# Performance work log

Measured on AMD Instinct MI355X. Metric: run time of the kernel, lower is better.

The kernel has to match this reference:

```python
import jax, jax.numpy as jnp
import numpy as np

B, SENSORY, STATE, MOTOR = 4096, 64, 128, 32
ODE_UNFOLDS = 6
EPS = 1e-8
ELAPSED_TIME = 1.0


def setup_inputs() -> dict:
    key = jax.random.key(0)
    ks = jax.random.split(key, 20)
    u = lambda k, shape, lo, hi: jax.random.uniform(k, shape, jnp.float32, lo, hi)
    sign = lambda k, shape: jnp.where(jax.random.bernoulli(k, 0.5, shape), 1.0, -1.0).astype(jnp.float32)
    mask = lambda k, shape: (jax.random.uniform(k, shape) < 0.75).astype(jnp.float32)
    return {
        "inputs": jax.random.normal(ks[0], (B, SENSORY), jnp.float32),
        "states": jax.random.normal(ks[1], (B, STATE), jnp.float32),
        "gleak": u(ks[2], (STATE,), 0.001, 1.0),
        "vleak": u(ks[3], (STATE,), -0.2, 0.2),
        "cm": u(ks[4], (STATE,), 0.4, 0.6),
        "w": u(ks[5], (STATE, STATE), 0.001, 1.0),
        "sigma": u(ks[6], (STATE, STATE), 3.0, 8.0),
        "mu": u(ks[7], (STATE, STATE), 0.3, 0.8),
        "erev": sign(ks[8], (STATE, STATE)),
        "sensory_w": u(ks[9], (SENSORY, STATE), 0.001, 1.0),
        "sensory_sigma": u(ks[10], (SENSORY, STATE), 3.0, 8.0),
        "sensory_mu": u(ks[11], (SENSORY, STATE), 0.3, 0.8),
        "sensory_erev": sign(ks[12], (SENSORY, STATE)),
        "sparsity_mask": mask(ks[13], (STATE, STATE)),
        "sensory_sparsity_mask": mask(ks[14], (SENSORY, STATE)),
        "input_w": jnp.ones((SENSORY,), jnp.float32),
        "input_b": jnp.zeros((SENSORY,), jnp.float32),
        "output_w": jnp.ones((MOTOR,), jnp.float32),
        "output_b": jnp.zeros((MOTOR,), jnp.float32),
    }


def _syn_sigmoid(v_pre, mu, sigma):
    # v_pre: [B, P] -> [B, P, 1]; mu/sigma: [P, S]
    return jax.nn.sigmoid(sigma * (v_pre[..., None] - mu))


def reference(inputs, states, gleak, vleak, cm, w, sigma, mu, erev,
              sensory_w, sensory_sigma, sensory_mu, sensory_erev,
              sparsity_mask, sensory_sparsity_mask,
              input_w, input_b, output_w, output_b):
    # input mapping (affine); make_positive_fn = Identity (explicit constraints)
    x = inputs * input_w + input_b

    # sensory contributions (computed once, shared across unfolds)
    sens_act = sensory_w * _syn_sigmoid(x, sensory_mu, sensory_sigma)  # [B, In, S]
    sens_act = sens_act * sensory_sparsity_mask
    w_num_sensory = jnp.sum(sens_act * sensory_erev, axis=1)  # [B, S]
    w_den_sensory = jnp.sum(sens_act, axis=1)                 # [B, S]

    cm_t = cm / (ELAPSED_TIME / ODE_UNFOLDS)  # [S]

    v_pre = states
    for _ in range(ODE_UNFOLDS):
        w_act = w * _syn_sigmoid(v_pre, mu, sigma)   # [B, S, S]
        w_act = w_act * sparsity_mask
        w_numerator = jnp.sum(w_act * erev, axis=1) + w_num_sensory
        w_denominator = jnp.sum(w_act, axis=1) + w_den_sensory
        numerator = cm_t * v_pre + gleak * vleak + w_numerator
        denominator = cm_t + gleak + w_denominator
        v_pre = numerator / (denominator + EPS)

    # output mapping: slice motor neurons, then affine
    output = v_pre[:, :MOTOR] * output_w + output_b
    return output, v_pre
```

## Files before the change

### kernel.cpp

```cpp
#include <hip/hip_runtime.h>

#define LOG2E 1.4426950408889634f

constexpr int Bsz = 4096, Ssz = 128, Isz = 64, MOTOR = 32;
constexpr int BT = 8, R = 4, NT = 512, NQ = 4;

__global__ void ltc_prep(const float* __restrict__ w, const float* __restrict__ sigma,
                         const float* __restrict__ mu, const float* __restrict__ erev,
                         const float* __restrict__ smask,
                         const float* __restrict__ sw, const float* __restrict__ ssig,
                         const float* __restrict__ smu, const float* __restrict__ serev,
                         const float* __restrict__ ssmask,
                         float4* __restrict__ A4, float4* __restrict__ B4, float4* __restrict__ W4,
                         float4* __restrict__ A4s, float4* __restrict__ B4s, float4* __restrict__ W4s)
{
  int idx = blockIdx.x * blockDim.x + threadIdx.x;
  if (idx < (Ssz / 4) * Ssz) {
    int j4 = idx >> 7, s = idx & 127;
    float4 a, b, wv;
    #pragma unroll
    for (int jj = 0; jj < 4; ++jj) {
      int e = (j4 * 4 + jj) * Ssz + s;
      float sg = sigma[e];
      (&a.x)[jj] = -sg * LOG2E;
      (&b.x)[jj] = sg * mu[e] * LOG2E;
      (&wv.x)[jj] = w[e] * smask[e] * erev[e];
    }
    A4[idx] = a; B4[idx] = b; W4[idx] = wv;
  } else if (idx < (Ssz / 4) * Ssz + (Isz / 4) * Ssz) {
    int k = idx - (Ssz / 4) * Ssz;
    int i4 = k >> 7, s = k & 127;
    float4 a, b, wv;
    #pragma unroll
    for (int jj = 0; jj < 4; ++jj) {
      int e = (i4 * 4 + jj) * Ssz + s;
      float sg = ssig[e];
      (&a.x)[jj] = -sg * LOG2E;
      (&b.x)[jj] = sg * smu[e] * LOG2E;
      (&wv.x)[jj] = sw[e] * ssmask[e] * serev[e];
    }
    A4s[k] = a; B4s[k] = b; W4s[k] = wv;
  }
}

__launch_bounds__(NT, 2)
__global__ void ltc_main(const float* __restrict__ inputs, const float* __restrict__ states,
                         const float* __restrict__ gleak, const float* __restrict__ vleak,
                         const float* __restrict__ cmv,
                         const float* __restrict__ iw, const float* __restrict__ ib,
                         const float* __restrict__ ow, const float* __restrict__ ob,
                         const float4* __restrict__ A4, const float4* __restrict__ B4,
                         const float4* __restrict__ W4,
                         const float4* __restrict__ A4s, const float4* __restrict__ B4s,
                         const float4* __restrict__ W4s,
                         float* __restrict__ out)
{
  __shared__ float vsh[BT][Ssz];
  __shared__ float xsh[BT][Isz];
  __shared__ float redn[NQ][R][Ssz];
  __shared__ float redd[NQ][R][Ssz];

  const int t = threadIdx.x;
  const int s = t & 127;
  const int qt = t >> 7;
  const int b0 = blockIdx.x * BT;

  for (int k = t; k < BT * Isz; k += NT) {
    int r = k >> 6, i = k & 63;
    xsh[r][i] = inputs[(b0 + r) * Isz + i] * iw[i] + ib[i];
  }
  for (int k = t; k < BT * Ssz; k += NT) {
    int r = k >> 7, ss = k & 127;
    vsh[r][ss] = states[(b0 + r) * Ssz + ss];
  }
  const float cmt = cmv[s] * 6.0f;
  const float gl = gleak[s];
  const float gv = gl * vleak[s];
  const float dbase = cmt + gl + 1e-8f;

  float4 ta[8], tb[8], tw[8];
  {
    const float4* Ab = A4 + (qt * 8) * Ssz + s;
    const float4* Bb = B4 + (qt * 8) * Ssz + s;
    const float4* Wb = W4 + (qt * 8) * Ssz + s;
    #pragma unroll
    for (int q = 0; q < 8; ++q) {
      ta[q] = Ab[q * Ssz];
      tb[q] = Bb[q * Ssz];
      tw[q] = Wb[q * Ssz];
    }
  }
  __syncthreads();

  #pragma unroll 1
  for (int cb = 0; cb < BT; cb += R) {
    float sn[R] = {0.f, 0.f, 0.f, 0.f}, sd[R] = {0.f, 0.f, 0.f, 0.f};
    #pragma unroll
    for (int q = 0; q < 4; ++q) {
      int iq = qt * 4 + q;
      float4 a4 = A4s[iq * Ssz + s];
      float4 b4 = B4s[iq * Ssz + s];
      float4 w4 = W4s[iq * Ssz + s];
      float4 xq[R];
      #pragma unroll
      for (int r = 0; r < R; ++r) xq[r] = *(const float4*)&xsh[cb + r][iq * 4];
      #pragma unroll
      for (int jj = 0; jj < 4; ++jj) {
        float av = (&a4.x)[jj], bv = (&b4.x)[jj], wv = (&w4.x)[jj];
        #pragma unroll
        for (int r = 0; r < R; ++r) {
          float arg = fmaf(av, (&xq[r].x)[jj], bv);
          float u = __builtin_amdgcn_exp2f(arg);
          float sig = __builtin_amdgcn_rcpf(1.0f + u);
          sn[r] = fmaf(wv, sig, sn[r]);
          sd[r] = fmaf(fabsf(wv), sig, sd[r]);
        }
      }
    }

    #pragma unroll 1
    for (int it = 0; it < 6; ++it) {
      float num[R], den[R];
      #pragma unroll
      for (int r = 0; r < R; ++r) { num[r] = sn[r]; den[r] = sd[r]; }

      #pragma unroll
      for (int q8 = 0; q8 < 8; ++q8) {
        float4 vc[R];
        #pragma unroll
        for (int r = 0; r < R; ++r) vc[r] = *(const float4*)&vsh[cb + r][qt * 32 + q8 * 4];
        #pragma unroll
        for (int jj = 0; jj < 4; ++jj) {
          float av = (&ta[q8].x)[jj], bv = (&tb[q8].x)[jj], wv = (&tw[q8].x)[jj];
          #pragma unroll
          for (int r = 0; r < R; ++r) {
            float arg = fmaf(av, (&vc[r].x)[jj], bv);
            float u = __builtin_amdgcn_exp2f(arg);
            float sig = __builtin_amdgcn_rcpf(1.0f + u);
            num[r] = fmaf(wv, sig, num[r]);
            den[r] = fmaf(fabsf(wv), sig, den[r]);
          }
        }
      }

      #pragma unroll
      for (int r = 0; r < R; ++r) { redn[qt][r][s] = num[r]; redd[qt][r][s] = den[r]; }
      __syncthreads();
      float fn = redn[0][qt][s] + redn[1][qt][s] + redn[2][qt][s] + redn[3][qt][s];
      float fd = redd[0][qt][s] + redd[1][qt][s] + redd[2][qt][s] + redd[3][qt][s];
      float vo = vsh[cb + qt][s];
      float nn = fmaf(cmt, vo, gv) + fn;
      float dd = dbase + fd;
      vsh[cb + qt][s] = nn * __builtin_amdgcn_rcpf(dd);
      __syncthreads();
    }
  }

  for (int k = t; k < BT * Ssz; k += NT) {
    int r = k >> 7, ss = k & 127;
    out[Bsz * MOTOR + (b0 + r) * Ssz + ss] = vsh[r][ss];
  }
  for (int k = t; k < BT * MOTOR; k += NT) {
    int r = k >> 5, m = k & 31;
    out[(b0 + r) * MOTOR + m] = fmaf(vsh[r][m], ow[m], ob[m]);
  }
}

extern "C" void kernel_launch(void* const* d_in, const int* in_sizes, int n_in,
                              void* d_out, int out_size, void* d_ws, size_t ws_size,
                              hipStream_t stream) {
  const float* inputs = (const float*)d_in[0];
  const float* states = (const float*)d_in[1];
  const float* gleak  = (const float*)d_in[2];
  const float* vleak  = (const float*)d_in[3];
  const float* cmv    = (const float*)d_in[4];
  const float* w      = (const float*)d_in[5];
  const float* sigma  = (const float*)d_in[6];
  const float* mu     = (const float*)d_in[7];
  const float* erev   = (const float*)d_in[8];
  const float* sw     = (const float*)d_in[9];
  const float* ssig   = (const float*)d_in[10];
  const float* smu    = (const float*)d_in[11];
  const float* serev  = (const float*)d_in[12];
  const float* smask  = (const float*)d_in[13];
  const float* ssmask = (const float*)d_in[14];
  const float* iw     = (const float*)d_in[15];
  const float* ib     = (const float*)d_in[16];
  const float* ow     = (const float*)d_in[17];
  const float* ob     = (const float*)d_in[18];

  char* ws = (char*)d_ws;
  float4* A4  = (float4*)(ws);
  float4* B4  = (float4*)(ws + 65536);
  float4* W4  = (float4*)(ws + 131072);
  float4* A4s = (float4*)(ws + 196608);
  float4* B4s = (float4*)(ws + 229376);
  float4* W4s = (float4*)(ws + 262144);
  float* out = (float*)d_out;

  constexpr int prep_items = (Ssz / 4) * Ssz + (Isz / 4) * Ssz;
  ltc_prep<<<(prep_items + 255) / 256, 256, 0, stream>>>(
      w, sigma, mu, erev, smask, sw, ssig, smu, serev, ssmask, A4, B4, W4, A4s, B4s, W4s);
  ltc_main<<<Bsz / BT, NT, 0, stream>>>(
      inputs, states, gleak, vleak, cmv, iw, ib, ow, ob, A4, B4, W4, A4s, B4s, W4s, out);
}
```

Baseline: 116.3 us.

## Stream interleaved synapse params from cache instead of holding them in registers

The main kernel now uses 4 rows per block with 256 threads split into two halves over presynaptic neurons, instead of 8 rows with 512 threads split four ways. The per-synapse A/B/W coefficients, previously held in 96 registers, are re-read from an interleaved global table (a, b, w adjacent per quad) on every unfold, which frees registers so launch bounds can allow 8 blocks per SM. The cross-half reduction becomes a two-way exchange in which each half finalises two rows. The trade is higher occupancy and a lighter reduction against repeated L1/L2 reads of the parameter table on every iteration.

```diff
diff --git a/kernel.cpp b/kernel.cpp
--- a/kernel.cpp
+++ b/kernel.cpp
@@ -3,7 +3,7 @@
 #define LOG2E 1.4426950408889634f
 
 constexpr int Bsz = 4096, Ssz = 128, Isz = 64, MOTOR = 32;
-constexpr int BT = 8, R = 4, NT = 512, NQ = 4;
+constexpr int BT = 4, NT = 256;
 
 __global__ void ltc_prep(const float* __restrict__ w, const float* __restrict__ sigma,
                          const float* __restrict__ mu, const float* __restrict__ erev,
@@ -11,64 +11,62 @@
                          const float* __restrict__ sw, const float* __restrict__ ssig,
                          const float* __restrict__ smu, const float* __restrict__ serev,
                          const float* __restrict__ ssmask,
-                         float4* __restrict__ A4, float4* __restrict__ B4, float4* __restrict__ W4,
-                         float4* __restrict__ A4s, float4* __restrict__ B4s, float4* __restrict__ W4s)
+                         float4* __restrict__ Tm, float4* __restrict__ Ts)
 {
   int idx = blockIdx.x * blockDim.x + threadIdx.x;
-  if (idx < (Ssz / 4) * Ssz) {
-    int j4 = idx >> 7, s = idx & 127;
+  if (idx < 32 * Ssz) {
+    int q = idx >> 7, s = idx & 127;
     float4 a, b, wv;
     #pragma unroll
     for (int jj = 0; jj < 4; ++jj) {
-      int e = (j4 * 4 + jj) * Ssz + s;
+      int e = (q * 4 + jj) * Ssz + s;
       float sg = sigma[e];
       (&a.x)[jj] = -sg * LOG2E;
       (&b.x)[jj] = sg * mu[e] * LOG2E;
       (&wv.x)[jj] = w[e] * smask[e] * erev[e];
     }
-    A4[idx] = a; B4[idx] = b; W4[idx] = wv;
-  } else if (idx < (Ssz / 4) * Ssz + (Isz / 4) * Ssz) {
-    int k = idx - (Ssz / 4) * Ssz;
-    int i4 = k >> 7, s = k & 127;
+    Tm[(q * 3 + 0) * Ssz + s] = a;
+    Tm[(q * 3 + 1) * Ssz + s] = b;
+    Tm[(q * 3 + 2) * Ssz + s] = wv;
+  } else if (idx < 32 * Ssz + 16 * Ssz) {
+    int k = idx - 32 * Ssz;
+    int q = k >> 7, s = k & 127;
     float4 a, b, wv;
     #pragma unroll
     for (int jj = 0; jj < 4; ++jj) {
-      int e = (i4 * 4 + jj) * Ssz + s;
+      int e = (q * 4 + jj) * Ssz + s;
       float sg = ssig[e];
       (&a.x)[jj] = -sg * LOG2E;
       (&b.x)[jj] = sg * smu[e] * LOG2E;
       (&wv.x)[jj] = sw[e] * ssmask[e] * serev[e];
     }
-    A4s[k] = a; B4s[k] = b; W4s[k] = wv;
+    Ts[(q * 3 + 0) * Ssz + s] = a;
+    Ts[(q * 3 + 1) * Ssz + s] = b;
+    Ts[(q * 3 + 2) * Ssz + s] = wv;
   }
 }
 
-__launch_bounds__(NT, 2)
+__launch_bounds__(NT, 8)
 __global__ void ltc_main(const float* __restrict__ inputs, const float* __restrict__ states,
                          const float* __restrict__ gleak, const float* __restrict__ vleak,
                          const float* __restrict__ cmv,
                          const float* __restrict__ iw, const float* __restrict__ ib,
                          const float* __restrict__ ow, const float* __restrict__ ob,
-                         const float4* __restrict__ A4, const float4* __restrict__ B4,
-                         const float4* __restrict__ W4,
-                         const float4* __restrict__ A4s, const float4* __restrict__ B4s,
-                         const float4* __restrict__ W4s,
+                         const float4* __restrict__ Tm, const float4* __restrict__ Ts,
                          float* __restrict__ out)
 {
   __shared__ float vsh[BT][Ssz];
   __shared__ float xsh[BT][Isz];
-  __shared__ float redn[NQ][R][Ssz];
-  __shared__ float redd[NQ][R][Ssz];
+  __shared__ float redn[2][2][Ssz];
+  __shared__ float redd[2][2][Ssz];
 
   const int t = threadIdx.x;
   const int s = t & 127;
-  const int qt = t >> 7;
+  const int h = t >> 7;
   const int b0 = blockIdx.x * BT;
 
-  for (int k = t; k < BT * Isz; k += NT) {
-    int r = k >> 6, i = k & 63;
-    xsh[r][i] = inputs[(b0 + r) * Isz + i] * iw[i] + ib[i];
-  }
+  { int r = t >> 6, i = t & 63;
+    xsh[r][i] = inputs[(b0 + r) * Isz + i] * iw[i] + ib[i]; }
   for (int k = t; k < BT * Ssz; k += NT) {
     int r = k >> 7, ss = k & 127;
     vsh[r][ss] = states[(b0 + r) * Ssz + ss];
@@ -77,91 +75,77 @@
   const float gl = gleak[s];
   const float gv = gl * vleak[s];
   const float dbase = cmt + gl + 1e-8f;
+  __syncthreads();
 
-  float4 ta[8], tb[8], tw[8];
+  float sn[BT] = {0.f, 0.f, 0.f, 0.f}, sd[BT] = {0.f, 0.f, 0.f, 0.f};
   {
-    const float4* Ab = A4 + (qt * 8) * Ssz + s;
-    const float4* Bb = B4 + (qt * 8) * Ssz + s;
-    const float4* Wb = W4 + (qt * 8) * Ssz + s;
-    #pragma unroll
+    const float4* pb = Ts + (h * 8 * 3 + 1) * Ssz + s;
+    #pragma unroll 2
     for (int q = 0; q < 8; ++q) {
-      ta[q] = Ab[q * Ssz];
-      tb[q] = Bb[q * Ssz];
-      tw[q] = Wb[q * Ssz];
+      float4 a4 = pb[-Ssz], b4 = pb[0], w4 = pb[Ssz];
+      pb += 3 * Ssz;
+      int col = (h * 8 + q) * 4;
+      #pragma unroll
+      for (int r = 0; r < BT; ++r) {
+        float4 xq = *(const float4*)&xsh[r][col];
+        #pragma unroll
+        for (int jj = 0; jj < 4; ++jj) {
+          float arg = fmaf((&a4.x)[jj], (&xq.x)[jj], (&b4.x)[jj]);
+          float u = __builtin_amdgcn_exp2f(arg);
+          float sig = __builtin_amdgcn_rcpf(1.0f + u);
+          sn[r] = fmaf((&w4.x)[jj], sig, sn[r]);
+          sd[r] = fmaf(fabsf((&w4.x)[jj]), sig, sd[r]);
+        }
+      }
     }
   }
-  __syncthreads();
 
   #pragma unroll 1
-  for (int cb = 0; cb < BT; cb += R) {
-    float sn[R] = {0.f, 0.f, 0.f, 0.f}, sd[R] = {0.f, 0.f, 0.f, 0.f};
+  for (int it = 0; it < 6; ++it) {
+    float num[BT], den[BT];
     #pragma unroll
-    for (int q = 0; q < 4; ++q) {
-      int iq = qt * 4 + q;
-      float4 a4 = A4s[iq * Ssz + s];
-      float4 b4 = B4s[iq * Ssz + s];
-      float4 w4 = W4s[iq * Ssz + s];
-      float4 xq[R];
+    for (int r = 0; r < BT; ++r) { num[r] = sn[r]; den[r] = sd[r]; }
+
+    const float4* pb = Tm + (h * 16 * 3 + 1) * Ssz + s;
+    #pragma unroll 2
+    for (int q = 0; q < 16; ++q) {
+      float4 a4 = pb[-Ssz], b4 = pb[0], w4 = pb[Ssz];
+      pb += 3 * Ssz;
+      int col = (h * 16 + q) * 4;
       #pragma unroll
-      for (int r = 0; r < R; ++r) xq[r] = *(const float4*)&xsh[cb + r][iq * 4];
-      #pragma unroll
-      for (int jj = 0; jj < 4; ++jj) {
-        float av = (&a4.x)[jj], bv = (&b4.x)[jj], wv = (&w4.x)[jj];
+      for (int r = 0; r < BT; ++r) {
+        float4 vq = *(const float4*)&vsh[r][col];
         #pragma unroll
-        for (int r = 0; r < R; ++r) {
-          float arg = fmaf(av, (&xq[r].x)[jj], bv);
+        for (int jj = 0; jj < 4; ++jj) {
+          float arg = fmaf((&a4.x)[jj], (&vq.x)[jj], (&b4.x)[jj]);
           float u = __builtin_amdgcn_exp2f(arg);
           float sig = __builtin_amdgcn_rcpf(1.0f + u);
-          sn[r] = fmaf(wv, sig, sn[r]);
-          sd[r] = fmaf(fabsf(wv), sig, sd[r]);
+          num[r] = fmaf((&w4.x)[jj], sig, num[r]);
+          den[r] = fmaf(fabsf((&w4.x)[jj]), sig, den[r]);
         }
       }
     }
 
-    #pragma unroll 1
-    for (int it = 0; it < 6; ++it) {
-      float num[R], den[R];
-      #pragma unroll
-      for (int r = 0; r < R; ++r) { num[r] = sn[r]; den[r] = sd[r]; }
-
-      #pragma unroll
-      for (int q8 = 0; q8 < 8; ++q8) {
-        float4 vc[R];
-        #pragma unroll
-        for (int r = 0; r < R; ++r) vc[r] = *(const float4*)&vsh[cb + r][qt * 32 + q8 * 4];
-        #pragma unroll
-        for (int jj = 0; jj < 4; ++jj) {
-          float av = (&ta[q8].x)[jj], bv = (&tb[q8].x)[jj], wv = (&tw[q8].x)[jj];
-          #pragma unroll
-          for (int r = 0; r < R; ++r) {
-            float arg = fmaf(av, (&vc[r].x)[jj], bv);
-            float u = __builtin_amdgcn_exp2f(arg);
-            float sig = __builtin_amdgcn_rcpf(1.0f + u);
-            num[r] = fmaf(wv, sig, num[r]);
-            den[r] = fmaf(fabsf(wv), sig, den[r]);
-          }
-        }
-      }
-
-      #pragma unroll
-      for (int r = 0; r < R; ++r) { redn[qt][r][s] = num[r]; redd[qt][r][s] = den[r]; }
-      __syncthreads();
-      float fn = redn[0][qt][s] + redn[1][qt][s] + redn[2][qt][s] + redn[3][qt][s];
-      float fd = redd[0][qt][s] + redd[1][qt][s] + redd[2][qt][s] + redd[3][qt][s];
-      float vo = vsh[cb + qt][s];
-      float nn = fmaf(cmt, vo, gv) + fn;
-      float dd = dbase + fd;
-      vsh[cb + qt][s] = nn * __builtin_amdgcn_rcpf(dd);
-      __syncthreads();
+    redn[h][0][s] = num[2 - 2 * h]; redn[h][1][s] = num[3 - 2 * h];
+    redd[h][0][s] = den[2 - 2 * h]; redd[h][1][s] = den[3 - 2 * h];
+    __syncthreads();
+    #pragma unroll
+    for (int k2 = 0; k2 < 2; ++k2) {
+      int r = 2 * h + k2;
+      float fn = num[r] + redn[1 - h][k2][s];
+      float fd = den[r] + redd[1 - h][k2][s];
+      float vo = vsh[r][s];
+      vsh[r][s] = (fmaf(cmt, vo, gv) + fn) * __builtin_amdgcn_rcpf(dbase + fd);
     }
+    __syncthreads();
   }
 
   for (int k = t; k < BT * Ssz; k += NT) {
     int r = k >> 7, ss = k & 127;
     out[Bsz * MOTOR + (b0 + r) * Ssz + ss] = vsh[r][ss];
   }
-  for (int k = t; k < BT * MOTOR; k += NT) {
-    int r = k >> 5, m = k & 31;
+  if (t < BT * MOTOR) {
+    int r = t >> 5, m = t & 31;
     out[(b0 + r) * MOTOR + m] = fmaf(vsh[r][m], ow[m], ob[m]);
   }
 }
@@ -190,17 +174,13 @@
   const float* ob     = (const float*)d_in[18];
 
   char* ws = (char*)d_ws;
-  float4* A4  = (float4*)(ws);
-  float4* B4  = (float4*)(ws + 65536);
-  float4* W4  = (float4*)(ws + 131072);
-  float4* A4s = (float4*)(ws + 196608);
-  float4* B4s = (float4*)(ws + 229376);
-  float4* W4s = (float4*)(ws + 262144);
+  float4* Tm = (float4*)ws;
+  float4* Ts = (float4*)(ws + 196608);
   float* out = (float*)d_out;
 
-  constexpr int prep_items = (Ssz / 4) * Ssz + (Isz / 4) * Ssz;
+  constexpr int prep_items = 32 * Ssz + 16 * Ssz;
   ltc_prep<<<(prep_items + 255) / 256, 256, 0, stream>>>(
-      w, sigma, mu, erev, smask, sw, ssig, smu, serev, ssmask, A4, B4, W4, A4s, B4s, W4s);
+      w, sigma, mu, erev, smask, sw, ssig, smu, serev, ssmask, Tm, Ts);
   ltc_main<<<Bsz / BT, NT, 0, stream>>>(
-      inputs, states, gleak, vleak, cmv, iw, ib, ow, ob, A4, B4, W4, A4s, B4s, W4s, out);
+      inputs, states, gleak, vleak, cmv, iw, ib, ow, ob, Tm, Ts, out);
 }
```

Result: slower. 119.5 us (+2.8%).
